# Kernel optimization log

Hardware: AMD Instinct MI355X
Metric: run time of the kernel (lower is better)

Reference implementation:

```python
import jax, jax.numpy as jnp
import numpy as np

B, IN_DIM, T = 4, 512, 4096
EMBED, HEADS, NB_FEAT = 1024, 16, 256
D_HEAD = EMBED // HEADS
EPS = 1e-6


def _orthogonal_random_matrix(key, nb_rows, nb_cols):
    # scaling==1 branch: sqrt(nb_cols) * Q from reduced QR of a Gaussian block
    block = jax.random.normal(key, (nb_rows, nb_cols), dtype=jnp.float32)
    q, _ = jnp.linalg.qr(block)
    return jnp.sqrt(jnp.float32(nb_cols)) * q


def setup_inputs() -> dict:
    key = jax.random.key(0)
    kx, kq, kk, kv, ko, kp = jax.random.split(key, 6)
    s = 1.0 / np.sqrt(IN_DIM)
    return {
        "x": jax.random.normal(kx, (B, IN_DIM, T), dtype=jnp.float32),
        "Wq": jax.random.normal(kq, (IN_DIM, EMBED), dtype=jnp.float32) * s,
        "Wk": jax.random.normal(kk, (IN_DIM, EMBED), dtype=jnp.float32) * s,
        "Wv": jax.random.normal(kv, (IN_DIM, EMBED), dtype=jnp.float32) * s,
        "Wo": jax.random.normal(ko, (EMBED, EMBED), dtype=jnp.float32) * (1.0 / np.sqrt(EMBED)),
        "proj": _orthogonal_random_matrix(kp, NB_FEAT, D_HEAD),
    }


def reference(x, Wq, Wk, Wv, Wo, proj):
    b, c, t = x.shape
    x_bt = jnp.transpose(x, (0, 2, 1))  # (B, T, in_dim)
    Q = (x_bt @ Wq).reshape(b, t, HEADS, D_HEAD)
    K = (x_bt @ Wk).reshape(b, t, HEADS, D_HEAD)
    V = (x_bt @ Wv).reshape(b, t, HEADS, D_HEAD)
    # exponential random-feature map
    Qp = jnp.exp(jnp.einsum('bthd,fd->bthf', Q, proj)) + EPS
    Kp = jnp.exp(jnp.einsum('bthd,fd->bthf', K, proj)) + EPS
    K_sum = Kp.sum(axis=1)                              # (B, H, F)
    KV = jnp.einsum('bthf,bthd->bhfd', Kp, V)           # (B, H, F, D)
    denom = jnp.maximum(jnp.einsum('bthf,bhf->bth', Qp, K_sum), 1e-6)
    numer = jnp.einsum('bthf,bhfd->bthd', Qp, KV)
    attn = numer / denom[..., None]                     # (B, T, H, D)
    out2 = attn.reshape(b, t, HEADS * D_HEAD) @ Wo      # (B, T, embed)
    cat = jnp.concatenate([x_bt, out2], axis=-1)        # (B, T, in_dim+embed)
    return jnp.transpose(cat, (0, 2, 1))
```

## Files before the change

kernel.cpp:

```cpp
#include <hip/hip_runtime.h>


constexpr int kB  = 4;
constexpr int kIn = 512;
constexpr int kT  = 4096;
constexpr int kE  = 1024;
constexpr int kH  = 16;
constexpr int kD  = 64;
constexpr int kF  = 256;
constexpr int kQKVs = 3072;

typedef __attribute__((ext_vector_type(8))) short bf16x8;
typedef __attribute__((ext_vector_type(4))) float f32x4;

__device__ __forceinline__ unsigned short f2bf(float f) {
    unsigned u = __float_as_uint(f);
    u += 0x7fff + ((u >> 16) & 1);
    return (unsigned short)(u >> 16);
}
__device__ __forceinline__ float bf2f(unsigned short s) {
    return __uint_as_float(((unsigned)s) << 16);
}
__device__ __forceinline__ void gload_lds16(const void* g, void* l) {
    __builtin_amdgcn_global_load_lds((const __attribute__((address_space(1))) void*)g,
                                     (__attribute__((address_space(3))) void*)l, 16, 0, 0);
}

__global__ __launch_bounds__(256) void zero_kernel(float* __restrict__ p, int n) {
    int i = blockIdx.x * 256 + threadIdx.x;
    if (i < n) p[i] = 0.f;
}

__global__ __launch_bounds__(256) void copy_x_kernel(const float* __restrict__ x,
                                                     float* __restrict__ out) {
    const int perB4 = kIn * kT / 4;
    int idx = blockIdx.x * 256 + threadIdx.x;
    if (idx < kB * perB4) {
        int b = idx / perB4, e = idx % perB4;
        ((float4*)out)[(size_t)b * ((kIn + kE) * kT / 4) + e] = ((const float4*)x)[idx];
    }
}

__global__ __launch_bounds__(256) void f2b_flat_kernel(const float* __restrict__ s,
                                                       unsigned short* __restrict__ d, int n4) {
    int i = blockIdx.x * 256 + threadIdx.x;
    if (i < n4) {
        float4 v = ((const float4*)s)[i];
        ushort4 o;
        o.x = f2bf(v.x); o.y = f2bf(v.y); o.z = f2bf(v.z); o.w = f2bf(v.w);
        ((ushort4*)d)[i] = o;
    }
}

__global__ __launch_bounds__(256) void trans_f2b_kernel(const float* __restrict__ src,
                                                        unsigned short* __restrict__ dst,
                                                        int R, int C,
                                                        long sstride, long dstride) {
    __shared__ float L[64][68];
    src += (size_t)blockIdx.z * sstride;
    dst += (size_t)blockIdx.z * dstride;
    const int c0 = blockIdx.x * 64, r0 = blockIdx.y * 64;
    const int tid = threadIdx.x;
#pragma unroll
    for (int it = 0; it < 4; ++it) {
        int lin = it * 256 + tid;
        int i = lin >> 4;
        int j4 = (lin & 15) * 4;
        float4 v = *(const float4*)(src + (size_t)(r0 + i) * C + c0 + j4);
        L[j4 + 0][i] = v.x; L[j4 + 1][i] = v.y; L[j4 + 2][i] = v.z; L[j4 + 3][i] = v.w;
    }
    __syncthreads();
#pragma unroll
    for (int it = 0; it < 4; ++it) {
        int lin = it * 256 + tid;
        int cc = lin >> 4;
        int r4 = (lin & 15) * 4;
        ushort4 o;
        o.x = f2bf(L[cc][r4 + 0]); o.y = f2bf(L[cc][r4 + 1]);
        o.z = f2bf(L[cc][r4 + 2]); o.w = f2bf(L[cc][r4 + 3]);
        *(ushort4*)(dst + (size_t)(c0 + cc) * R + r0 + r4) = o;
    }
}

__global__ __launch_bounds__(256) void trans_qkv_kernel(const float* __restrict__ Wq,
                                                        const float* __restrict__ Wk,
                                                        const float* __restrict__ Wv,
                                                        unsigned short* __restrict__ dst) {
    __shared__ float L[64][68];
    const int z = blockIdx.z;
    const float* src = (z == 0) ? Wq : (z == 1) ? Wk : Wv;
    dst += (size_t)z * kE * kIn;
    const int c0 = blockIdx.x * 64, r0 = blockIdx.y * 64;
    const int tid = threadIdx.x;
#pragma unroll
    for (int it = 0; it < 4; ++it) {
        int lin = it * 256 + tid;
        int i = lin >> 4;
        int j4 = (lin & 15) * 4;
        float4 v = *(const float4*)(src + (size_t)(r0 + i) * kE + c0 + j4);
        L[j4 + 0][i] = v.x; L[j4 + 1][i] = v.y; L[j4 + 2][i] = v.z; L[j4 + 3][i] = v.w;
    }
    __syncthreads();
#pragma unroll
    for (int it = 0; it < 4; ++it) {
        int lin = it * 256 + tid;
        int cc = lin >> 4;
        int r4 = (lin & 15) * 4;
        ushort4 o;
        o.x = f2bf(L[cc][r4 + 0]); o.y = f2bf(L[cc][r4 + 1]);
        o.z = f2bf(L[cc][r4 + 2]); o.w = f2bf(L[cc][r4 + 3]);
        *(ushort4*)(dst + (size_t)(c0 + cc) * kIn + r0 + r4) = o;
    }
}

__device__ __forceinline__ void gemm128_mainloop(const unsigned short* __restrict__ A,
                                                 const unsigned short* __restrict__ Bt,
                                                 int K, int m0, int n0,
                                                 unsigned short* As, unsigned short* Bs,
                                                 f32x4 (&acc)[4][4]) {
    const int tid = threadIdx.x, lane = tid & 63, w = tid >> 6;
    const int col = lane & 15, quad = lane >> 4;
    const int wm = (w >> 2) * 64, wn = (w & 3) * 64;
    const int nt = K >> 5;

    const unsigned short* Agl  = A  + (size_t)(m0 + (tid >> 2)) * K + (tid & 3) * 8;
    const unsigned short* Bgl0 = Bt + (size_t)(n0 + (tid >> 2)) * K + (tid & 3) * 8;
    const unsigned short* Bgl1 = Bgl0 + (size_t)128 * K;
    unsigned short* Asw = As + w * 512;
    unsigned short* Bsw = Bs + w * 512;

    auto stage = [&](int kt, int buf) {
        gload_lds16(Agl  + kt * 32, Asw + buf * 4096);
        gload_lds16(Bgl0 + kt * 32, Bsw + buf * 8192);
        gload_lds16(Bgl1 + kt * 32, Bsw + buf * 8192 + 4096);
    };

#pragma unroll
    for (int i = 0; i < 4; ++i)
#pragma unroll
        for (int j = 0; j < 4; ++j) acc[i][j] = (f32x4){0.f, 0.f, 0.f, 0.f};

    stage(0, 0);
    if (nt > 1) stage(1, 1);
    asm volatile("s_waitcnt vmcnt(3)" ::: "memory");
    __builtin_amdgcn_s_barrier();
    __builtin_amdgcn_sched_barrier(0);

    for (int t = 0; t < nt; ++t) {
        const int cur = t & 1;
        const unsigned short* Ab = As + cur * 4096;
        const unsigned short* Bb = Bs + cur * 8192;
        bf16x8 av[4], bv[4];
#pragma unroll
        for (int i = 0; i < 4; ++i)
            av[i] = *(const bf16x8*)&Ab[(wm + i * 16 + col) * 32 + quad * 8];
#pragma unroll
        for (int j = 0; j < 4; ++j)
            bv[j] = *(const bf16x8*)&Bb[(wn + j * 16 + col) * 32 + quad * 8];
        asm volatile("s_waitcnt lgkmcnt(0)" ::: "memory");
        __builtin_amdgcn_sched_barrier(0);
        __builtin_amdgcn_s_barrier();
        if (t + 2 < nt) stage(t + 2, cur);
        __builtin_amdgcn_sched_barrier(0);
#pragma unroll
        for (int i = 0; i < 4; ++i)
#pragma unroll
            for (int j = 0; j < 4; ++j)
                acc[i][j] = __builtin_amdgcn_mfma_f32_16x16x32_bf16(av[i], bv[j], acc[i][j], 0, 0, 0);
        if (t + 1 < nt) {
            __builtin_amdgcn_sched_barrier(0);
            if (t + 2 < nt) asm volatile("s_waitcnt vmcnt(3)" ::: "memory");
            else            asm volatile("s_waitcnt vmcnt(0)" ::: "memory");
            __builtin_amdgcn_sched_barrier(0);
            __builtin_amdgcn_s_barrier();
            __builtin_amdgcn_sched_barrier(0);
        }
    }
}

__global__ __launch_bounds__(512, 4) void gemm128_b16(const unsigned short* __restrict__ A,
                                                      const unsigned short* __restrict__ Bt,
                                                      unsigned short* __restrict__ C,
                                                      int N, int K, int ntN) {
    __shared__ unsigned short As[2 * 4096];
    __shared__ unsigned short Bs[2 * 8192];
    __shared__ float Tt[8][336];
    const int tid = threadIdx.x, lane = tid & 63, w = tid >> 6;
    const int col = lane & 15, quad = lane >> 4;
    const int wm = (w >> 2) * 64, wn = (w & 3) * 64;
    const int bid = blockIdx.x;
    const int qch = gridDim.x >> 3;
    const int swb = (bid & 7) * qch + (bid >> 3);
    const int mt = swb / ntN, ntl = swb - mt * ntN;
    const int m0 = mt * 128, n0 = ntl * 256;

    f32x4 acc[4][4];
    gemm128_mainloop(A, Bt, K, m0, n0, As, Bs, acc);

    float* Tw = Tt[w];
    const int t2 = lane >> 2, n4 = (lane & 3) * 4;
#pragma unroll
    for (int ri = 0; ri < 4; ++ri)
#pragma unroll
        for (int cj = 0; cj < 4; ++cj) {
#pragma unroll
            for (int r = 0; r < 4; ++r)
                Tw[(quad * 4 + r) * 20 + col] = acc[ri][cj][r];
            float4 v = *(const float4*)&Tw[t2 * 20 + n4];
            ushort4 o;
            o.x = f2bf(v.x); o.y = f2bf(v.y); o.z = f2bf(v.z); o.w = f2bf(v.w);
            *(ushort4*)(C + (size_t)(m0 + wm + ri * 16 + t2) * N + n0 + wn + cj * 16 + n4) = o;
        }
}

__global__ __launch_bounds__(512, 4) void gemm128_out(const unsigned short* __restrict__ A,
                                                      const unsigned short* __restrict__ Bt,
                                                      float* __restrict__ out,
                                                      int N, int K, int ntN) {
    __shared__ unsigned short As[2 * 4096];
    __shared__ unsigned short Bs[2 * 8192];
    __shared__ float Tt[8][336];
    const int tid = threadIdx.x, lane = tid & 63, w = tid >> 6;
    const int col = lane & 15, quad = lane >> 4;
    const int wm = (w >> 2) * 64, wn = (w & 3) * 64;
    const int bid = blockIdx.x;
    const int qch = gridDim.x >> 3;
    const int swb = (bid & 7) * qch + (bid >> 3);
    const int mt = swb / ntN, ntl = swb - mt * ntN;
    const int m0 = mt * 128, n0 = ntl * 256;

    f32x4 acc[4][4];
    gemm128_mainloop(A, Bt, K, m0, n0, As, Bs, acc);

    const int b = m0 >> 12, t0 = m0 & 4095;
    float* dst = out + (size_t)b * (kIn + kE) * kT + (size_t)kIn * kT;
    float* Tw = Tt[w];
    const int n2 = lane >> 2, t4 = (lane & 3) * 4;
#pragma unroll
    for (int ri = 0; ri < 4; ++ri)
#pragma unroll
        for (int cj = 0; cj < 4; ++cj) {
            *(float4*)&Tw[col * 20 + quad * 4] =
                (float4){acc[ri][cj][0], acc[ri][cj][1], acc[ri][cj][2], acc[ri][cj][3]};
            float4 v = *(const float4*)&Tw[n2 * 20 + t4];
            *(float4*)(dst + (size_t)(n0 + wn + cj * 16 + n2) * kT + t0 + wm + ri * 16 + t4) = v;
        }
}

__global__ __launch_bounds__(256) void phaseA_mfma(const unsigned short* __restrict__ QKVb,
                                                   const unsigned short* __restrict__ projb,
                                                   float* __restrict__ KVg,
                                                   float* __restrict__ Ksumg) {
    __shared__ unsigned short Ks[64 * 64];
    __shared__ unsigned short VT[64 * 72];
    __shared__ unsigned short KpT[256 * 72];
    const int tid = threadIdx.x, lane = tid & 63, w = tid >> 6;
    const int col = lane & 15, quad = lane >> 4;
    const int bh = blockIdx.x, b = bh >> 4, h = bh & 15;
    const int grp = blockIdx.y;
    const int f0 = w * 64;
    const int swz = col & 7;

    bf16x8 bB[2][4];
#pragma unroll
    for (int s = 0; s < 2; ++s)
#pragma unroll
        for (int j = 0; j < 4; ++j)
            bB[s][j] = *(const bf16x8*)(projb + (size_t)(f0 + j * 16 + col) * 64 + s * 32 + quad * 8);

    f32x4 kvacc[4][4];
#pragma unroll
    for (int i = 0; i < 4; ++i)
#pragma unroll
        for (int j = 0; j < 4; ++j) kvacc[i][j] = (f32x4){0.f, 0.f, 0.f, 0.f};
    float ksum_acc[4] = {0.f, 0.f, 0.f, 0.f};

    for (int it = 0; it < 8; ++it) {
        const size_t rowbase = (size_t)(b * kT + grp * 512 + it * 64) * kQKVs + h * kD;
        __syncthreads();
#pragma unroll
        for (int i2 = 0; i2 < 2; ++i2) {
            int p = (i2 * 4 + w) * 64 + lane;
            int row = p >> 3;
            int cg = ((p & 7) ^ (row & 7)) * 8;
            gload_lds16(QKVb + rowbase + 1024 + (size_t)row * kQKVs + cg, &Ks[(i2 * 4 + w) * 512]);
        }
#pragma unroll
        for (int r = 0; r < 4; ++r) {
            int lin = r * 256 + tid;
            int t = lin >> 4, d4 = (lin & 15) * 4;
            ushort4 v = *(const ushort4*)(QKVb + rowbase + 2048 + (size_t)t * kQKVs + d4);
            VT[(d4 + 0) * 72 + t] = v.x; VT[(d4 + 1) * 72 + t] = v.y;
            VT[(d4 + 2) * 72 + t] = v.z; VT[(d4 + 3) * 72 + t] = v.w;
        }
        __syncthreads();
        bf16x8 av[2][4];
#pragma unroll
        for (int s = 0; s < 2; ++s)
#pragma unroll
            for (int i = 0; i < 4; ++i)
                av[s][i] = *(const bf16x8*)&Ks[(i * 16 + col) * 64 + ((s * 4 + quad) ^ swz) * 8];
#pragma unroll
        for (int j = 0; j < 4; ++j) {
            f32x4 sa[4];
#pragma unroll
            for (int i = 0; i < 4; ++i) sa[i] = (f32x4){0.f, 0.f, 0.f, 0.f};
#pragma unroll
            for (int s = 0; s < 2; ++s)
#pragma unroll
                for (int i = 0; i < 4; ++i)
                    sa[i] = __builtin_amdgcn_mfma_f32_16x16x32_bf16(av[s][i], bB[s][j], sa[i], 0, 0, 0);
            const int f = f0 + j * 16 + col;
#pragma unroll
            for (int i = 0; i < 4; ++i) {
                float e0 = __expf(sa[i][0]) + 1e-6f;
                float e1 = __expf(sa[i][1]) + 1e-6f;
                float e2 = __expf(sa[i][2]) + 1e-6f;
                float e3 = __expf(sa[i][3]) + 1e-6f;
                ksum_acc[j] += (e0 + e1) + (e2 + e3);
                ushort4 pk;
                pk.x = f2bf(e0); pk.y = f2bf(e1); pk.z = f2bf(e2); pk.w = f2bf(e3);
                *(ushort4*)&KpT[f * 72 + i * 16 + quad * 4] = pk;
            }
        }
#pragma unroll
        for (int s = 0; s < 2; ++s) {
            const int kc = s * 32 + quad * 8;
            bf16x8 a2[4], b2[4];
#pragma unroll
            for (int i = 0; i < 4; ++i)
                a2[i] = *(const bf16x8*)&KpT[(f0 + i * 16 + col) * 72 + kc];
#pragma unroll
            for (int jn = 0; jn < 4; ++jn)
                b2[jn] = *(const bf16x8*)&VT[(jn * 16 + col) * 72 + kc];
#pragma unroll
            for (int i = 0; i < 4; ++i)
#pragma unroll
                for (int jn = 0; jn < 4; ++jn)
                    kvacc[i][jn] = __builtin_amdgcn_mfma_f32_16x16x32_bf16(a2[i], b2[jn], kvacc[i][jn], 0, 0, 0);
        }
    }
    const size_t kvbase = (size_t)bh * (kF * kD);
#pragma unroll
    for (int i = 0; i < 4; ++i)
#pragma unroll
        for (int jn = 0; jn < 4; ++jn)
#pragma unroll
            for (int r = 0; r < 4; ++r)
                atomicAdd(&KVg[kvbase + (size_t)(f0 + i * 16 + quad * 4 + r) * kD + jn * 16 + col],
                          kvacc[i][jn][r]);
#pragma unroll
    for (int j = 0; j < 4; ++j) {
        float v = ksum_acc[j];
        v += __shfl_xor(v, 16);
        v += __shfl_xor(v, 32);
        if (quad == 0) atomicAdd(&Ksumg[(size_t)bh * kF + f0 + j * 16 + col], v);
    }
}

__global__ __launch_bounds__(256) void phaseB_mfma(const unsigned short* __restrict__ QKVb,
                                                   const unsigned short* __restrict__ projb,
                                                   const unsigned short* __restrict__ KVTb,
                                                   const float* __restrict__ Ksumg,
                                                   unsigned short* __restrict__ attnb) {
    __shared__ unsigned short Qs[64 * 64];
    __shared__ unsigned short Qp[64 * 264];
    __shared__ unsigned short KVTs[64 * 264];
    __shared__ float KsS[256];
    __shared__ float denp[4][64];
    const int tid = threadIdx.x, lane = tid & 63, w = tid >> 6;
    const int col = lane & 15, quad = lane >> 4;
    const int bh = blockIdx.x, b = bh >> 4, h = bh & 15;
    const int grp = blockIdx.y;
    const int f0 = w * 64;
    const int swz = col & 7;

    bf16x8 bB[2][4];
#pragma unroll
    for (int s = 0; s < 2; ++s)
#pragma unroll
        for (int j = 0; j < 4; ++j)
            bB[s][j] = *(const bf16x8*)(projb + (size_t)(f0 + j * 16 + col) * 64 + s * 32 + quad * 8);

#pragma unroll
    for (int r = 0; r < 8; ++r) {
        int lin = r * 256 + tid;
        int d = lin >> 5, fc8 = (lin & 31) * 8;
        *(bf16x8*)&KVTs[d * 264 + fc8] = *(const bf16x8*)(KVTb + (size_t)bh * 16384 + d * 256 + fc8);
    }
    KsS[tid] = Ksumg[(size_t)bh * kF + tid];

    for (int it = 0; it < 8; ++it) {
        const int tg0 = grp * 512 + it * 64;
        const size_t rowbase = (size_t)(b * kT + tg0) * kQKVs + h * kD;
        __syncthreads();
#pragma unroll
        for (int i2 = 0; i2 < 2; ++i2) {
            int p = (i2 * 4 + w) * 64 + lane;
            int row = p >> 3;
            int cg = ((p & 7) ^ (row & 7)) * 8;
            gload_lds16(QKVb + rowbase + (size_t)row * kQKVs + cg, &Qs[(i2 * 4 + w) * 512]);
        }
        __syncthreads();
        bf16x8 av[2][4];
#pragma unroll
        for (int s = 0; s < 2; ++s)
#pragma unroll
            for (int i = 0; i < 4; ++i)
                av[s][i] = *(const bf16x8*)&Qs[(i * 16 + col) * 64 + ((s * 4 + quad) ^ swz) * 8];
#pragma unroll
        for (int j = 0; j < 4; ++j) {
            f32x4 sa[4];
#pragma unroll
            for (int i = 0; i < 4; ++i) sa[i] = (f32x4){0.f, 0.f, 0.f, 0.f};
#pragma unroll
            for (int s = 0; s < 2; ++s)
#pragma unroll
                for (int i = 0; i < 4; ++i)
                    sa[i] = __builtin_amdgcn_mfma_f32_16x16x32_bf16(av[s][i], bB[s][j], sa[i], 0, 0, 0);
            const int f = f0 + j * 16 + col;
#pragma unroll
            for (int i = 0; i < 4; ++i) {
                const int tb = i * 16 + quad * 4;
                Qp[(tb + 0) * 264 + f] = f2bf(__expf(sa[i][0]) + 1e-6f);
                Qp[(tb + 1) * 264 + f] = f2bf(__expf(sa[i][1]) + 1e-6f);
                Qp[(tb + 2) * 264 + f] = f2bf(__expf(sa[i][2]) + 1e-6f);
                Qp[(tb + 3) * 264 + f] = f2bf(__expf(sa[i][3]) + 1e-6f);
            }
        }
        float dp = 0.f;
#pragma unroll
        for (int u = 0; u < 64; u += 8) {
            bf16x8 qv = *(const bf16x8*)&Qp[lane * 264 + f0 + u];
#pragma unroll
            for (int k2 = 0; k2 < 8; ++k2)
                dp += bf2f((unsigned short)qv[k2]) * KsS[f0 + u + k2];
        }
        denp[w][lane] = dp;
        __syncthreads();
        f32x4 nacc[4];
#pragma unroll
        for (int jn = 0; jn < 4; ++jn) nacc[jn] = (f32x4){0.f, 0.f, 0.f, 0.f};
#pragma unroll
        for (int s = 0; s < 8; ++s) {
            const int kc = s * 32 + quad * 8;
            bf16x8 aq = *(const bf16x8*)&Qp[(w * 16 + col) * 264 + kc];
#pragma unroll
            for (int jn = 0; jn < 4; ++jn) {
                bf16x8 bk = *(const bf16x8*)&KVTs[(jn * 16 + col) * 264 + kc];
                nacc[jn] = __builtin_amdgcn_mfma_f32_16x16x32_bf16(aq, bk, nacc[jn], 0, 0, 0);
            }
        }
#pragma unroll
        for (int r = 0; r < 4; ++r) {
            const int tl = w * 16 + quad * 4 + r;
            float den = denp[0][tl] + denp[1][tl] + denp[2][tl] + denp[3][tl];
            float rd = 1.f / fmaxf(den, 1e-6f);
            const size_t ob = (size_t)(b * kT + tg0 + tl) * kE + h * kD;
#pragma unroll
            for (int jn = 0; jn < 4; ++jn)
                attnb[ob + jn * 16 + col] = f2bf(nacc[jn][r] * rd);
        }
    }
}

extern "C" void kernel_launch(void* const* d_in, const int* in_sizes, int n_in,
                              void* d_out, int out_size, void* d_ws, size_t ws_size,
                              hipStream_t stream) {
    (void)in_sizes; (void)n_in; (void)out_size; (void)ws_size;
    const float* x    = (const float*)d_in[0];
    const float* Wq   = (const float*)d_in[1];
    const float* Wk   = (const float*)d_in[2];
    const float* Wv   = (const float*)d_in[3];
    const float* Wo   = (const float*)d_in[4];
    const float* proj = (const float*)d_in[5];
    float* out = (float*)d_out;

    char* ws = (char*)d_ws;
    unsigned short* QKVb  = (unsigned short*)(ws);
    unsigned short* attnb = (unsigned short*)(ws + 100663296);
    unsigned short* Abuf  = (unsigned short*)(ws + 100663296);
    unsigned short* Btqkv = (unsigned short*)(ws + 134217728);
    unsigned short* WoT   = (unsigned short*)(ws + 137363456);
    unsigned short* projb = (unsigned short*)(ws + 139460608);
    float*          KVg   = (float*)(ws + 139493376);
    float*          Ksumg = (float*)(ws + 143687680);
    unsigned short* KVTb  = (unsigned short*)(ws + 143753216);

    copy_x_kernel<<<dim3(8192), 256, 0, stream>>>(x, out);

    trans_f2b_kernel<<<dim3(64, 8, 4), 256, 0, stream>>>(x, Abuf, kIn, kT,
                                                         (long)kIn * kT, (long)kT * kIn);
    trans_qkv_kernel<<<dim3(16, 8, 3), 256, 0, stream>>>(Wq, Wk, Wv, Btqkv);
    trans_f2b_kernel<<<dim3(16, 16, 1), 256, 0, stream>>>(Wo, WoT, kE, kE, 0, 0);
    f2b_flat_kernel<<<dim3(16), 256, 0, stream>>>(proj, projb, kF * kD / 4);

    gemm128_b16<<<dim3(1536), 512, 0, stream>>>(Abuf, Btqkv, QKVb, kQKVs, kIn, 12);

    const int nz = kB * kH * kF * kD + kB * kH * kF;
    zero_kernel<<<dim3((nz + 255) / 256), 256, 0, stream>>>(KVg, nz);

    phaseA_mfma<<<dim3(64, 8), 256, 0, stream>>>(QKVb, projb, KVg, Ksumg);
    trans_f2b_kernel<<<dim3(1, 4, 64), 256, 0, stream>>>(KVg, KVTb, kF, kD,
                                                         (long)kF * kD, (long)kF * kD);
    phaseB_mfma<<<dim3(64, 8), 256, 0, stream>>>(QKVb, projb, KVTb, Ksumg, attnb);

    gemm128_out<<<dim3(512), 512, 0, stream>>>(attnb, WoT, out, kE, kE, 4);
}
```

Before: 374.2 us.

## Fuse x copy into transpose, swizzle GEMM LDS, reuse LDS for epilogue, split phaseA

Merges the x passthrough copy into the x transpose/bf16 conversion kernel, so x is read from global memory once instead of twice. Adds an XOR swizzle to the GEMM LDS staging and fragment reads to reduce bank conflicts. Reuses the A-tile LDS buffer for the epilogue transpose scratch, which lowers shared memory per block and may raise occupancy. Doubles the phaseA grid along T with half the iterations per block, giving more parallelism at the cost of more atomic accumulation into KV.

```diff
diff --git a/kernel.cpp b/kernel.cpp
--- a/kernel.cpp
+++ b/kernel.cpp
@@ -31,16 +31,6 @@
     if (i < n) p[i] = 0.f;
 }
 
-__global__ __launch_bounds__(256) void copy_x_kernel(const float* __restrict__ x,
-                                                     float* __restrict__ out) {
-    const int perB4 = kIn * kT / 4;
-    int idx = blockIdx.x * 256 + threadIdx.x;
-    if (idx < kB * perB4) {
-        int b = idx / perB4, e = idx % perB4;
-        ((float4*)out)[(size_t)b * ((kIn + kE) * kT / 4) + e] = ((const float4*)x)[idx];
-    }
-}
-
 __global__ __launch_bounds__(256) void f2b_flat_kernel(const float* __restrict__ s,
                                                        unsigned short* __restrict__ d, int n4) {
     int i = blockIdx.x * 256 + threadIdx.x;
@@ -49,6 +39,38 @@
         ushort4 o;
         o.x = f2bf(v.x); o.y = f2bf(v.y); o.z = f2bf(v.z); o.w = f2bf(v.w);
         ((ushort4*)d)[i] = o;
+    }
+}
+
+__global__ __launch_bounds__(256) void trans_xcopy_kernel(const float* __restrict__ x,
+                                                          float* __restrict__ out,
+                                                          unsigned short* __restrict__ dst) {
+    __shared__ float L[64][68];
+    const int b = blockIdx.z;
+    const float* src = x + (size_t)b * kIn * kT;
+    float4* outb = (float4*)out + (size_t)b * ((kIn + kE) * kT / 4);
+    unsigned short* dstb = dst + (size_t)b * kT * kIn;
+    const int c0 = blockIdx.x * 64, r0 = blockIdx.y * 64;
+    const int tid = threadIdx.x;
+#pragma unroll
+    for (int it = 0; it < 4; ++it) {
+        int lin = it * 256 + tid;
+        int i = lin >> 4;
+        int j4 = (lin & 15) * 4;
+        float4 v = *(const float4*)(src + (size_t)(r0 + i) * kT + c0 + j4);
+        outb[((size_t)(r0 + i) * kT + c0 + j4) >> 2] = v;
+        L[j4 + 0][i] = v.x; L[j4 + 1][i] = v.y; L[j4 + 2][i] = v.z; L[j4 + 3][i] = v.w;
+    }
+    __syncthreads();
+#pragma unroll
+    for (int it = 0; it < 4; ++it) {
+        int lin = it * 256 + tid;
+        int cc = lin >> 4;
+        int r4 = (lin & 15) * 4;
+        ushort4 o;
+        o.x = f2bf(L[cc][r4 + 0]); o.y = f2bf(L[cc][r4 + 1]);
+        o.z = f2bf(L[cc][r4 + 2]); o.w = f2bf(L[cc][r4 + 3]);
+        *(ushort4*)(dstb + (size_t)(c0 + cc) * kIn + r0 + r4) = o;
     }
 }
 
@@ -123,8 +145,10 @@
     const int wm = (w >> 2) * 64, wn = (w & 3) * 64;
     const int nt = K >> 5;
 
-    const unsigned short* Agl  = A  + (size_t)(m0 + (tid >> 2)) * K + (tid & 3) * 8;
-    const unsigned short* Bgl0 = Bt + (size_t)(n0 + (tid >> 2)) * K + (tid & 3) * 8;
+    const int srow = tid >> 2;
+    const int schk = (tid & 3) ^ ((tid >> 3) & 3);
+    const unsigned short* Agl  = A  + (size_t)(m0 + srow) * K + schk * 8;
+    const unsigned short* Bgl0 = Bt + (size_t)(n0 + srow) * K + schk * 8;
     const unsigned short* Bgl1 = Bgl0 + (size_t)128 * K;
     unsigned short* Asw = As + w * 512;
     unsigned short* Bsw = Bs + w * 512;
@@ -146,6 +170,8 @@
     __builtin_amdgcn_s_barrier();
     __builtin_amdgcn_sched_barrier(0);
 
+    const int rchk = (quad ^ ((col >> 1) & 3)) * 8;
+
     for (int t = 0; t < nt; ++t) {
         const int cur = t & 1;
         const unsigned short* Ab = As + cur * 4096;
@@ -153,10 +179,10 @@
         bf16x8 av[4], bv[4];
 #pragma unroll
         for (int i = 0; i < 4; ++i)
-            av[i] = *(const bf16x8*)&Ab[(wm + i * 16 + col) * 32 + quad * 8];
+            av[i] = *(const bf16x8*)&Ab[(wm + i * 16 + col) * 32 + rchk];
 #pragma unroll
         for (int j = 0; j < 4; ++j)
-            bv[j] = *(const bf16x8*)&Bb[(wn + j * 16 + col) * 32 + quad * 8];
+            bv[j] = *(const bf16x8*)&Bb[(wn + j * 16 + col) * 32 + rchk];
         asm volatile("s_waitcnt lgkmcnt(0)" ::: "memory");
         __builtin_amdgcn_sched_barrier(0);
         __builtin_amdgcn_s_barrier();
@@ -184,7 +210,6 @@
                                                       int N, int K, int ntN) {
     __shared__ unsigned short As[2 * 4096];
     __shared__ unsigned short Bs[2 * 8192];
-    __shared__ float Tt[8][336];
     const int tid = threadIdx.x, lane = tid & 63, w = tid >> 6;
     const int col = lane & 15, quad = lane >> 4;
     const int wm = (w >> 2) * 64, wn = (w & 3) * 64;
@@ -197,7 +222,7 @@
     f32x4 acc[4][4];
     gemm128_mainloop(A, Bt, K, m0, n0, As, Bs, acc);
 
-    float* Tw = Tt[w];
+    float* Tw = (float*)As + w * 336;
     const int t2 = lane >> 2, n4 = (lane & 3) * 4;
 #pragma unroll
     for (int ri = 0; ri < 4; ++ri)
@@ -219,7 +244,6 @@
                                                       int N, int K, int ntN) {
     __shared__ unsigned short As[2 * 4096];
     __shared__ unsigned short Bs[2 * 8192];
-    __shared__ float Tt[8][336];
     const int tid = threadIdx.x, lane = tid & 63, w = tid >> 6;
     const int col = lane & 15, quad = lane >> 4;
     const int wm = (w >> 2) * 64, wn = (w & 3) * 64;
@@ -234,7 +258,7 @@
 
     const int b = m0 >> 12, t0 = m0 & 4095;
     float* dst = out + (size_t)b * (kIn + kE) * kT + (size_t)kIn * kT;
-    float* Tw = Tt[w];
+    float* Tw = (float*)As + w * 336;
     const int n2 = lane >> 2, t4 = (lane & 3) * 4;
 #pragma unroll
     for (int ri = 0; ri < 4; ++ri)
@@ -275,8 +299,8 @@
         for (int j = 0; j < 4; ++j) kvacc[i][j] = (f32x4){0.f, 0.f, 0.f, 0.f};
     float ksum_acc[4] = {0.f, 0.f, 0.f, 0.f};
 
-    for (int it = 0; it < 8; ++it) {
-        const size_t rowbase = (size_t)(b * kT + grp * 512 + it * 64) * kQKVs + h * kD;
+    for (int it = 0; it < 4; ++it) {
+        const size_t rowbase = (size_t)(b * kT + grp * 256 + it * 64) * kQKVs + h * kD;
         __syncthreads();
 #pragma unroll
         for (int i2 = 0; i2 < 2; ++i2) {
@@ -487,10 +511,7 @@
     float*          Ksumg = (float*)(ws + 143687680);
     unsigned short* KVTb  = (unsigned short*)(ws + 143753216);
 
-    copy_x_kernel<<<dim3(8192), 256, 0, stream>>>(x, out);
-
-    trans_f2b_kernel<<<dim3(64, 8, 4), 256, 0, stream>>>(x, Abuf, kIn, kT,
-                                                         (long)kIn * kT, (long)kT * kIn);
+    trans_xcopy_kernel<<<dim3(64, 8, 4), 256, 0, stream>>>(x, out, Abuf);
     trans_qkv_kernel<<<dim3(16, 8, 3), 256, 0, stream>>>(Wq, Wk, Wv, Btqkv);
     trans_f2b_kernel<<<dim3(16, 16, 1), 256, 0, stream>>>(Wo, WoT, kE, kE, 0, 0);
     f2b_flat_kernel<<<dim3(16), 256, 0, stream>>>(proj, projb, kF * kD / 4);
@@ -500,7 +521,7 @@
     const int nz = kB * kH * kF * kD + kB * kH * kF;
     zero_kernel<<<dim3((nz + 255) / 256), 256, 0, stream>>>(KVg, nz);
 
-    phaseA_mfma<<<dim3(64, 8), 256, 0, stream>>>(QKVb, projb, KVg, Ksumg);
+    phaseA_mfma<<<dim3(64, 16), 256, 0, stream>>>(QKVb, projb, KVg, Ksumg);
     trans_f2b_kernel<<<dim3(1, 4, 64), 256, 0, stream>>>(KVg, KVTb, kF, kD,
                                                          (long)kF * kD, (long)kF * kD);
     phaseB_mfma<<<dim3(64, 8), 256, 0, stream>>>(QKVb, projb, KVTb, Ksumg, attnb);
```

New measurement: 378.3 us. Within noise of the previous version (+1.1%).
